# Optimization experiments

Measured on AMD Instinct MI355X. Metric: run time of the kernel, lower is better.

The kernel has to match this reference:

```python
import jax, jax.numpy as jnp
import numpy as np

ATT_DIM = 768
N_HEADS = 4
N_LABELS = 2000
NEG_INF = -1e6


def setup_inputs() -> dict:
    key = jax.random.key(0)
    k1, k2, k3, k4, k5, k6 = jax.random.split(key, 6)
    B, S, D = 4, 3072, ATT_DIM
    h = jax.random.normal(k1, (B, S, D), dtype=jnp.float32)
    attention_mask = jnp.ones((B, S), dtype=jnp.int32)
    label_feat = jax.random.normal(k2, (N_LABELS * N_HEADS, D), dtype=jnp.float32)
    # nn.Linear W: weight [D, D], bias [D]
    W_w = jax.random.normal(k3, (D, D), dtype=jnp.float32) * 0.02
    W_b = jnp.zeros((D,), dtype=jnp.float32)
    # classifier: weight [num_labels, D], bias [num_labels]
    cls_w = jax.random.normal(k4, (N_LABELS, D), dtype=jnp.float32) * 0.02
    cls_b = jnp.zeros((N_LABELS,), dtype=jnp.float32)
    return {"h": h, "attention_mask": attention_mask, "label_feat": label_feat,
            "W_w": W_w, "W_b": W_b, "cls_w": cls_w, "cls_b": cls_b}


def reference(h, attention_mask, label_feat, W_w, W_b, cls_w, cls_b):
    # h: [B,S,D]; label_feat: [E*H, D]
    B, S, D = h.shape
    E = label_feat.shape[0] // N_HEADS
    z = jnp.tanh(h @ W_w.T + W_b)                       # [B,S,D]
    u = label_feat.reshape(E, N_HEADS, D)               # [E,H,D]
    # score 'abd,ecd->aebc' -> [B,E,S,H]
    score = jnp.einsum('bsd,ehd->besh', z, u)
    mask = attention_mask.astype(bool)[:, None, :, None]  # [B,1,S,1]
    score = jnp.where(mask, score, NEG_INF)
    alpha = jax.nn.softmax(score, axis=2)               # softmax over seq
    # m 'abd,aebc->aedc' -> [B,E,D,H]
    m = jnp.einsum('bsd,besh->bedh', h, alpha)
    m = m.max(axis=-1)                                  # head max-pool -> [B,E,D]
    logits = jnp.sum(cls_w[None] * m, axis=2) + cls_b   # [B,E]
    return logits, m
```

## Files before the change

kernel.cpp:

```cpp
#include <hip/hip_runtime.h>
#include <hip/hip_bf16.h>

typedef _Float16 f16;
typedef _Float16 half8 __attribute__((ext_vector_type(8)));
typedef _Float16 half4v __attribute__((ext_vector_type(4)));
typedef float f32x4 __attribute__((ext_vector_type(4)));

#define B_ 4
#define S_ 3072
#define D_ 768
#define E_ 2000
#define NEG_INF -1.0e6f

#define GLD16(gsrc, ldst)                                                     \
  __builtin_amdgcn_global_load_lds(                                           \
      (const __attribute__((address_space(1))) void*)(gsrc),                  \
      (__attribute__((address_space(3))) void*)(ldst), 16, 0, 0)

__global__ __launch_bounds__(256) void k_transpose(const float* __restrict__ h,
                                                   f16* __restrict__ ht) {
  __shared__ f16 tile[64][65];
  int b = blockIdx.z, s0 = blockIdx.x * 64, d0 = blockIdx.y * 64;
  int t = threadIdx.x, tx = t & 63, ty = t >> 6;
  const float* src = h + ((size_t)b * S_ + s0) * D_ + d0;
#pragma unroll
  for (int i = 0; i < 16; ++i) {
    int sl = i * 4 + ty;
    tile[sl][tx] = (f16)src[(size_t)sl * D_ + tx];
  }
  __syncthreads();
  f16* dst = ht + ((size_t)b * D_ + d0) * S_ + s0;
#pragma unroll
  for (int i = 0; i < 16; ++i) {
    int dl = i * 4 + ty;
    dst[(size_t)dl * S_ + tx] = tile[tx][dl];
  }
}

__global__ __launch_bounds__(256) void k_zgemm(const float* __restrict__ h,
                                               const float* __restrict__ W,
                                               const float* __restrict__ bias,
                                               f16* __restrict__ zb) {
  __shared__ f16 As[64][40];
  __shared__ f16 Bs[64][40];
  int i0 = blockIdx.x * 64, j0 = blockIdx.y * 64;
  int t = threadIdx.x, w = t >> 6, lane = t & 63, g = lane >> 4, li = lane & 15;
  int wi = w >> 1, wj = w & 1;

  f32x4 acc[2][2];
#pragma unroll
  for (int a = 0; a < 2; ++a)
#pragma unroll
    for (int b2 = 0; b2 < 2; ++b2) acc[a][b2] = (f32x4){0.f, 0.f, 0.f, 0.f};

  int srow = t >> 2, scol = (t & 3) * 8;
  const float* pA = h + (size_t)(i0 + srow) * D_ + scol;
  const float* pB = W + (size_t)(j0 + srow) * D_ + scol;

  for (int kc = 0; kc < D_; kc += 32) {
    float4 a0 = *(const float4*)(pA + kc);
    float4 a1 = *(const float4*)(pA + kc + 4);
    float4 b0 = *(const float4*)(pB + kc);
    float4 b1 = *(const float4*)(pB + kc + 4);
    half8 av = {(f16)a0.x, (f16)a0.y, (f16)a0.z, (f16)a0.w,
                (f16)a1.x, (f16)a1.y, (f16)a1.z, (f16)a1.w};
    half8 bv = {(f16)b0.x, (f16)b0.y, (f16)b0.z, (f16)b0.w,
                (f16)b1.x, (f16)b1.y, (f16)b1.z, (f16)b1.w};
    *(half8*)&As[srow][scol] = av;
    *(half8*)&Bs[srow][scol] = bv;
    __syncthreads();
#pragma unroll
    for (int it = 0; it < 2; ++it) {
      half8 af = *(const half8*)&As[wi * 32 + it * 16 + li][g * 8];
#pragma unroll
      for (int jt = 0; jt < 2; ++jt) {
        half8 bf = *(const half8*)&Bs[wj * 32 + jt * 16 + li][g * 8];
        acc[it][jt] =
            __builtin_amdgcn_mfma_f32_16x16x32_f16(af, bf, acc[it][jt], 0, 0, 0);
      }
    }
    __syncthreads();
  }
#pragma unroll
  for (int it = 0; it < 2; ++it) {
#pragma unroll
    for (int jt = 0; jt < 2; ++jt) {
      int jj = j0 + wj * 32 + jt * 16 + li;
      float bsv = bias[jj];
#pragma unroll
      for (int r = 0; r < 4; ++r) {
        int ii = i0 + wi * 32 + it * 16 + g * 4 + r;
        float v = acc[it][jt][r] + bsv;
        zb[(size_t)ii * D_ + jj] = (f16)tanhf(v);
      }
    }
  }
}

__global__ __launch_bounds__(512, 1) void k_attn(const float* __restrict__ lf,
                                                 const f16* __restrict__ zb,
                                                 const f16* __restrict__ ht,
                                                 const int* __restrict__ amask,
                                                 float* __restrict__ out_m) {
  __shared__ f16 KsBuf[2][32 * 768];
  __shared__ f16 VsBuf[768 * 32];
  __shared__ f16 PtBuf[64 * 32];
  __shared__ float Cp[32][68];
  __shared__ float Fac[64];
  __shared__ float Lfin[64];
  __shared__ int Msk[2][32];

  char* KsB = (char*)&KsBuf[0][0];
  char* VsB = (char*)VsBuf;
  char* PtB = (char*)PtBuf;

  const int fid = blockIdx.x;
  const int x2 = fid & 7, u = fid >> 3;
  const int b = x2 >> 1;
  const int qtile = (x2 & 1) * 64 + u;
  if (qtile >= 125) return;
  const int q0 = qtile * 64;

  const int t = threadIdx.x, w = t >> 6, lane = t & 63;
  const int g = lane >> 4, li = lane & 15;
  const int qt = w & 3, kh = w >> 2;
  const int dh = w;

  half8 qf[12];
  {
    const float* qp = lf + (size_t)(q0 + qt * 16 + li) * D_ + kh * 384 + g * 8;
#pragma unroll
    for (int f = 0; f < 12; ++f) {
      float4 v0 = *(const float4*)(qp + f * 32);
      float4 v1 = *(const float4*)(qp + f * 32 + 4);
      qf[f] = (half8){(f16)v0.x, (f16)v0.y, (f16)v0.z, (f16)v0.w,
                      (f16)v1.x, (f16)v1.y, (f16)v1.z, (f16)v1.w};
    }
  }

  int klds[6], kgsw[6];
#pragma unroll
  for (int k = 0; k < 6; ++k) {
    int lin = (w * 6 + k) * 1024 + lane * 16;
    int row = lin / 1536;
    int xo = lin - row * 1536;
    klds[k] = lin;
    kgsw[k] = row * 1536 + (xo ^ ((row & 7) << 4));
  }
  int vlds[6], vgsw[6];
#pragma unroll
  for (int k = 0; k < 6; ++k) {
    int j = w * 6 + k;
    int vd = j * 16 + (lane >> 2);
    vlds[k] = j * 1024 + lane * 16;
    vgsw[k] = vd * (S_ * 2) + (((lane & 3) * 16) ^ ((vd & 3) << 4));
  }

  const int amask7 = (li & 7) << 4;
  const int arow0 = li * 1536 + kh * 768;
  const int arow1 = (16 + li) * 1536 + kh * 768;

  const int vroff = (dh * 96 + li) * 64 + ((g * 16) ^ ((li & 3) << 4));
  int ptoff[4];
#pragma unroll
  for (int qs = 0; qs < 4; ++qs)
    ptoff[qs] = (qs * 16 + li) * 64 + ((g * 16) ^ ((li & 3) << 4));

  const int pwoff0 = (qt * 16 + li) * 64 + ((g * 8) ^ ((li & 3) << 4));
  const int pwoff1 = (qt * 16 + li) * 64 + ((32 + g * 8) ^ ((li & 3) << 4));

  const char* zbB = (const char*)zb + (size_t)b * S_ * 1536;
  const char* htB = (const char*)ht + (size_t)b * D_ * S_ * 2;

#pragma unroll
  for (int k = 0; k < 6; ++k) GLD16(zbB + kgsw[k], KsB + klds[k]);
  if (t < 32) Msk[0][t] = amask[b * S_ + t];
  asm volatile("s_waitcnt vmcnt(0)" ::: "memory");
  __syncthreads();

  float mreg = -3.0e38f, lreg = 0.0f;
  f32x4 oacc[4][6];
#pragma unroll
  for (int a = 0; a < 4; ++a)
#pragma unroll
    for (int d = 0; d < 6; ++d) oacc[a][d] = (f32x4){0.f, 0.f, 0.f, 0.f};

  for (int i = 0; i < 96; ++i) {
    const int s0 = i * 32;
    const int s0n = (i < 95) ? s0 + 32 : 0;
    const int cur = i & 1, nxt = cur ^ 1;
    const char* ksC = KsB + cur * 49152;

    int mnext = (t < 32) ? amask[b * S_ + s0n + t] : 0;
    {
      const char* src = htB + (size_t)s0 * 2;
#pragma unroll
      for (int k = 0; k < 6; ++k) GLD16(src + vgsw[k], VsB + vlds[k]);
    }

    f32x4 c0 = {0.f, 0.f, 0.f, 0.f}, c1 = {0.f, 0.f, 0.f, 0.f};
    f32x4 e0 = {0.f, 0.f, 0.f, 0.f}, e1 = {0.f, 0.f, 0.f, 0.f};
    __builtin_amdgcn_s_setprio(1);
#pragma unroll
    for (int kf = 0; kf < 6; ++kf) {
      const int col = (kf * 64 + g * 16) ^ amask7;
      half8 a0 = *(const half8*)(ksC + arow0 + col);
      half8 a1 = *(const half8*)(ksC + arow1 + col);
      c0 = __builtin_amdgcn_mfma_f32_16x16x32_f16(a0, qf[kf], c0, 0, 0, 0);
      c1 = __builtin_amdgcn_mfma_f32_16x16x32_f16(a1, qf[kf], c1, 0, 0, 0);
    }
#pragma unroll
    for (int kf = 6; kf < 12; ++kf) {
      const int col = (kf * 64 + g * 16) ^ amask7;
      half8 a0 = *(const half8*)(ksC + arow0 + col);
      half8 a1 = *(const half8*)(ksC + arow1 + col);
      e0 = __builtin_amdgcn_mfma_f32_16x16x32_f16(a0, qf[kf], e0, 0, 0, 0);
      e1 = __builtin_amdgcn_mfma_f32_16x16x32_f16(a1, qf[kf], e1, 0, 0, 0);
    }
    __builtin_amdgcn_s_setprio(0);
    c0 = c0 + e0;
    c1 = c1 + e1;

    __builtin_amdgcn_sched_barrier(0);
    {
      const char* src = zbB + (size_t)s0n * 1536;
      char* dst = KsB + nxt * 49152;
#pragma unroll
      for (int k = 0; k < 6; ++k) GLD16(src + kgsw[k], dst + klds[k]);
    }

    if (kh == 1) {
#pragma unroll
      for (int r = 0; r < 4; ++r) {
        Cp[g * 4 + r][qt * 16 + li] = c0[r];
        Cp[16 + g * 4 + r][qt * 16 + li] = c1[r];
      }
    }
    __syncthreads();

    if (kh == 0) {
      const int* mk = Msk[i & 1];
      float p[8];
      float vmax = -3.0e38f;
#pragma unroll
      for (int r = 0; r < 4; ++r) {
        float sv0 = c0[r] + Cp[g * 4 + r][qt * 16 + li];
        float sv1 = c1[r] + Cp[16 + g * 4 + r][qt * 16 + li];
        if (!mk[g * 4 + r]) sv0 = NEG_INF;
        if (!mk[16 + g * 4 + r]) sv1 = NEG_INF;
        p[r] = sv0;
        p[4 + r] = sv1;
        vmax = fmaxf(vmax, fmaxf(sv0, sv1));
      }
      vmax = fmaxf(vmax, __shfl_xor(vmax, 16));
      vmax = fmaxf(vmax, __shfl_xor(vmax, 32));
      float Mn = fmaxf(mreg, vmax);
      float fec = __expf(mreg - Mn);
      mreg = Mn;
      float ts = 0.f;
#pragma unroll
      for (int r = 0; r < 8; ++r) {
        p[r] = __expf(p[r] - Mn);
        ts += p[r];
      }
      ts += __shfl_xor(ts, 16);
      ts += __shfl_xor(ts, 32);
      lreg = lreg * fec + ts;
      if (lane < 16) Fac[qt * 16 + li] = fec;
      *(half4v*)(PtB + pwoff0) =
          (half4v){(f16)p[0], (f16)p[1], (f16)p[2], (f16)p[3]};
      *(half4v*)(PtB + pwoff1) =
          (half4v){(f16)p[4], (f16)p[5], (f16)p[6], (f16)p[7]};
    }
    if (t < 32) Msk[(i + 1) & 1][t] = mnext;
    asm volatile("s_waitcnt vmcnt(6)" ::: "memory");
    __syncthreads();

    {
      float fr[4][4];
#pragma unroll
      for (int qs = 0; qs < 4; ++qs)
#pragma unroll
        for (int r = 0; r < 4; ++r) fr[qs][r] = Fac[qs * 16 + g * 4 + r];
#pragma unroll
      for (int qs = 0; qs < 4; ++qs)
#pragma unroll
        for (int dt = 0; dt < 6; ++dt)
#pragma unroll
          for (int r = 0; r < 4; ++r) oacc[qs][dt][r] *= fr[qs][r];
      half8 pa[4];
#pragma unroll
      for (int qs = 0; qs < 4; ++qs) pa[qs] = *(const half8*)(PtB + ptoff[qs]);
      __builtin_amdgcn_s_setprio(1);
#pragma unroll
      for (int dt = 0; dt < 6; ++dt) {
        half8 vb = *(const half8*)(VsB + vroff + dt * 1024);
#pragma unroll
        for (int qs = 0; qs < 4; ++qs)
          oacc[qs][dt] =
              __builtin_amdgcn_mfma_f32_16x16x32_f16(pa[qs], vb, oacc[qs][dt], 0, 0, 0);
      }
      __builtin_amdgcn_s_setprio(0);
    }
    asm volatile("s_waitcnt vmcnt(0)" ::: "memory");
    __syncthreads();
  }

  if (kh == 0 && lane < 16) Lfin[qt * 16 + li] = lreg;
  __syncthreads();

#pragma unroll
  for (int qs = 0; qs < 4; ++qs) {
    float rl[4];
#pragma unroll
    for (int r = 0; r < 4; ++r) rl[r] = 1.0f / Lfin[qs * 16 + g * 4 + r];
    int e_loc = qs * 4 + g;
    float* od = out_m + ((size_t)b * E_ + (q0 >> 2) + e_loc) * D_ + dh * 96 + li;
#pragma unroll
    for (int dt = 0; dt < 6; ++dt) {
      float mv = oacc[qs][dt][0] * rl[0];
      mv = fmaxf(mv, oacc[qs][dt][1] * rl[1]);
      mv = fmaxf(mv, oacc[qs][dt][2] * rl[2]);
      mv = fmaxf(mv, oacc[qs][dt][3] * rl[3]);
      od[dt * 16] = mv;
    }
  }
}

__global__ __launch_bounds__(256) void k_logits(const float* __restrict__ cw,
                                                const float* __restrict__ cb,
                                                const float* __restrict__ m,
                                                float* __restrict__ out) {
  int t = threadIdx.x, w = t >> 6, lane = t & 63;
  int rid = blockIdx.x * 4 + w;
  int b = rid / E_, e = rid - b * E_;
  const float* mr = m + (size_t)rid * D_;
  const float* cr = cw + (size_t)e * D_;
  float acc = 0.f;
#pragma unroll
  for (int i = 0; i < 12; ++i) acc += cr[i * 64 + lane] * mr[i * 64 + lane];
#pragma unroll
  for (int off = 32; off >= 1; off >>= 1) acc += __shfl_xor(acc, off);
  if (lane == 0) out[rid] = acc + cb[e];
}

extern "C" void kernel_launch(void* const* d_in, const int* in_sizes, int n_in,
                              void* d_out, int out_size, void* d_ws, size_t ws_size,
                              hipStream_t stream) {
  const float* h = (const float*)d_in[0];
  const int* amask = (const int*)d_in[1];
  const float* lf = (const float*)d_in[2];
  const float* Ww = (const float*)d_in[3];
  const float* Wb = (const float*)d_in[4];
  const float* cw = (const float*)d_in[5];
  const float* cb = (const float*)d_in[6];
  float* out = (float*)d_out;

  f16* zb = (f16*)d_ws;
  f16* ht = (f16*)((char*)d_ws + 18874368);

  k_transpose<<<dim3(48, 12, 4), 256, 0, stream>>>(h, ht);
  k_zgemm<<<dim3(192, 12), 256, 0, stream>>>(h, Ww, Wb, zb);
  k_attn<<<512, 512, 0, stream>>>(lf, zb, ht, amask, out + 8000);
  k_logits<<<2000, 256, 0, stream>>>(cw, cb, out + 8000, out);
}
```

Baseline: 633.3 us.

## Load V fragments directly into registers and software-pipeline PV with next QK

Removes the shared-memory V staging buffer and loads each warp's ht fragments straight from global memory into double-buffered registers. The loop is restructured so the P·V MFMA for the previous tile runs at the start of the next iteration, before that iteration's QK^T, with a final drain after the loop. This drops one barrier per iteration, replaces __syncthreads with raw s_barrier plus explicit waitcnt, and changes the P-buffer swizzle. The aim is to hide V load latency and cut LDS traffic and synchronisation, at the cost of more VGPRs and uncoalesced, strided global loads for V.

```diff
diff --git a/kernel.cpp b/kernel.cpp
--- a/kernel.cpp
+++ b/kernel.cpp
@@ -103,7 +103,6 @@
                                                  const int* __restrict__ amask,
                                                  float* __restrict__ out_m) {
   __shared__ f16 KsBuf[2][32 * 768];
-  __shared__ f16 VsBuf[768 * 32];
   __shared__ f16 PtBuf[64 * 32];
   __shared__ float Cp[32][68];
   __shared__ float Fac[64];
@@ -111,7 +110,6 @@
   __shared__ int Msk[2][32];
 
   char* KsB = (char*)&KsBuf[0][0];
-  char* VsB = (char*)VsBuf;
   char* PtB = (char*)PtBuf;
 
   const int fid = blockIdx.x;
@@ -147,30 +145,21 @@
     klds[k] = lin;
     kgsw[k] = row * 1536 + (xo ^ ((row & 7) << 4));
   }
-  int vlds[6], vgsw[6];
-#pragma unroll
-  for (int k = 0; k < 6; ++k) {
-    int j = w * 6 + k;
-    int vd = j * 16 + (lane >> 2);
-    vlds[k] = j * 1024 + lane * 16;
-    vgsw[k] = vd * (S_ * 2) + (((lane & 3) * 16) ^ ((vd & 3) << 4));
-  }
 
   const int amask7 = (li & 7) << 4;
   const int arow0 = li * 1536 + kh * 768;
   const int arow1 = (16 + li) * 1536 + kh * 768;
 
-  const int vroff = (dh * 96 + li) * 64 + ((g * 16) ^ ((li & 3) << 4));
+  const int pswz = ((li >> 1) & 3) << 4;
   int ptoff[4];
 #pragma unroll
   for (int qs = 0; qs < 4; ++qs)
-    ptoff[qs] = (qs * 16 + li) * 64 + ((g * 16) ^ ((li & 3) << 4));
-
-  const int pwoff0 = (qt * 16 + li) * 64 + ((g * 8) ^ ((li & 3) << 4));
-  const int pwoff1 = (qt * 16 + li) * 64 + ((32 + g * 8) ^ ((li & 3) << 4));
+    ptoff[qs] = (qs * 16 + li) * 64 + ((g * 16) ^ pswz);
+  const int pwoff0 = (qt * 16 + li) * 64 + ((g * 8) ^ pswz);
+  const int pwoff1 = (qt * 16 + li) * 64 + ((32 + g * 8) ^ pswz);
 
   const char* zbB = (const char*)zb + (size_t)b * S_ * 1536;
-  const char* htB = (const char*)ht + (size_t)b * D_ * S_ * 2;
+  const f16* vbase = ht + ((size_t)b * D_ + dh * 96 + li) * S_ + g * 8;
 
 #pragma unroll
   for (int k = 0; k < 6; ++k) GLD16(zbB + kgsw[k], KsB + klds[k]);
@@ -185,125 +174,139 @@
 #pragma unroll
     for (int d = 0; d < 6; ++d) oacc[a][d] = (f32x4){0.f, 0.f, 0.f, 0.f};
 
-  for (int i = 0; i < 96; ++i) {
-    const int s0 = i * 32;
-    const int s0n = (i < 95) ? s0 + 32 : 0;
-    const int cur = i & 1, nxt = cur ^ 1;
-    const char* ksC = KsB + cur * 49152;
-
-    int mnext = (t < 32) ? amask[b * S_ + s0n + t] : 0;
-    {
-      const char* src = htB + (size_t)s0 * 2;
-#pragma unroll
-      for (int k = 0; k < 6; ++k) GLD16(src + vgsw[k], VsB + vlds[k]);
-    }
-
-    f32x4 c0 = {0.f, 0.f, 0.f, 0.f}, c1 = {0.f, 0.f, 0.f, 0.f};
-    f32x4 e0 = {0.f, 0.f, 0.f, 0.f}, e1 = {0.f, 0.f, 0.f, 0.f};
-    __builtin_amdgcn_s_setprio(1);
-#pragma unroll
-    for (int kf = 0; kf < 6; ++kf) {
-      const int col = (kf * 64 + g * 16) ^ amask7;
-      half8 a0 = *(const half8*)(ksC + arow0 + col);
-      half8 a1 = *(const half8*)(ksC + arow1 + col);
-      c0 = __builtin_amdgcn_mfma_f32_16x16x32_f16(a0, qf[kf], c0, 0, 0, 0);
-      c1 = __builtin_amdgcn_mfma_f32_16x16x32_f16(a1, qf[kf], c1, 0, 0, 0);
-    }
-#pragma unroll
-    for (int kf = 6; kf < 12; ++kf) {
-      const int col = (kf * 64 + g * 16) ^ amask7;
-      half8 a0 = *(const half8*)(ksC + arow0 + col);
-      half8 a1 = *(const half8*)(ksC + arow1 + col);
-      e0 = __builtin_amdgcn_mfma_f32_16x16x32_f16(a0, qf[kf], e0, 0, 0, 0);
-      e1 = __builtin_amdgcn_mfma_f32_16x16x32_f16(a1, qf[kf], e1, 0, 0, 0);
-    }
-    __builtin_amdgcn_s_setprio(0);
-    c0 = c0 + e0;
-    c1 = c1 + e1;
-
-    __builtin_amdgcn_sched_barrier(0);
-    {
-      const char* src = zbB + (size_t)s0n * 1536;
-      char* dst = KsB + nxt * 49152;
-#pragma unroll
-      for (int k = 0; k < 6; ++k) GLD16(src + kgsw[k], dst + klds[k]);
-    }
-
-    if (kh == 1) {
-#pragma unroll
-      for (int r = 0; r < 4; ++r) {
-        Cp[g * 4 + r][qt * 16 + li] = c0[r];
-        Cp[16 + g * 4 + r][qt * 16 + li] = c1[r];
-      }
-    }
-    __syncthreads();
-
-    if (kh == 0) {
-      const int* mk = Msk[i & 1];
-      float p[8];
-      float vmax = -3.0e38f;
-#pragma unroll
-      for (int r = 0; r < 4; ++r) {
-        float sv0 = c0[r] + Cp[g * 4 + r][qt * 16 + li];
-        float sv1 = c1[r] + Cp[16 + g * 4 + r][qt * 16 + li];
-        if (!mk[g * 4 + r]) sv0 = NEG_INF;
-        if (!mk[16 + g * 4 + r]) sv1 = NEG_INF;
-        p[r] = sv0;
-        p[4 + r] = sv1;
-        vmax = fmaxf(vmax, fmaxf(sv0, sv1));
-      }
-      vmax = fmaxf(vmax, __shfl_xor(vmax, 16));
-      vmax = fmaxf(vmax, __shfl_xor(vmax, 32));
-      float Mn = fmaxf(mreg, vmax);
-      float fec = __expf(mreg - Mn);
-      mreg = Mn;
-      float ts = 0.f;
-#pragma unroll
-      for (int r = 0; r < 8; ++r) {
-        p[r] = __expf(p[r] - Mn);
-        ts += p[r];
-      }
-      ts += __shfl_xor(ts, 16);
-      ts += __shfl_xor(ts, 32);
-      lreg = lreg * fec + ts;
-      if (lane < 16) Fac[qt * 16 + li] = fec;
-      *(half4v*)(PtB + pwoff0) =
-          (half4v){(f16)p[0], (f16)p[1], (f16)p[2], (f16)p[3]};
-      *(half4v*)(PtB + pwoff1) =
-          (half4v){(f16)p[4], (f16)p[5], (f16)p[6], (f16)p[7]};
-    }
-    if (t < 32) Msk[(i + 1) & 1][t] = mnext;
-    asm volatile("s_waitcnt vmcnt(6)" ::: "memory");
-    __syncthreads();
-
-    {
-      float fr[4][4];
+  half8 Vb0[6], Vb1[6];
+
+#define ATT_BODY(I_, VRD, VWR)                                                \
+  {                                                                           \
+    const int i_ = (I_);                                                      \
+    const int s0_ = i_ * 32;                                                  \
+    const int s0n_ = (i_ < 95) ? s0_ + 32 : 0;                                \
+    const char* ksC_ = KsB + (i_ & 1) * 49152;                                \
+    char* ksN_ = KsB + ((i_ & 1) ^ 1) * 49152;                                \
+    int mnext_ = (t < 32) ? amask[b * S_ + s0n_ + t] : 0;                     \
+    {                            \
+      const char* src_ = zbB + (size_t)s0n_ * 1536;                           \
+      _Pragma("unroll") for (int k = 0; k < 6; ++k)                           \
+          GLD16(src_ + kgsw[k], ksN_ + klds[k]);                              \
+    }                                                                         \
+    {                         \
+      const f16* vp_ = vbase + s0_;                                           \
+      _Pragma("unroll") for (int dt = 0; dt < 6; ++dt)                        \
+          VWR[dt] = *(const half8*)(vp_ + (size_t)dt * 16 * S_);              \
+    }                                                                         \
+    __builtin_amdgcn_sched_barrier(0);                                        \
+    if (i_ > 0) {                       \
+      float fr_[4][4];                                                        \
+      _Pragma("unroll") for (int qs = 0; qs < 4; ++qs)                        \
+          _Pragma("unroll") for (int r = 0; r < 4; ++r)                       \
+              fr_[qs][r] = Fac[qs * 16 + g * 4 + r];                          \
+      _Pragma("unroll") for (int qs = 0; qs < 4; ++qs)                        \
+          _Pragma("unroll") for (int dt = 0; dt < 6; ++dt)                    \
+              _Pragma("unroll") for (int r = 0; r < 4; ++r)                   \
+                  oacc[qs][dt][r] *= fr_[qs][r];                              \
+      half8 pa_[4];                                                           \
+      _Pragma("unroll") for (int qs = 0; qs < 4; ++qs)                        \
+          pa_[qs] = *(const half8*)(PtB + ptoff[qs]);                         \
+      __builtin_amdgcn_s_setprio(1);                                          \
+      _Pragma("unroll") for (int dt = 0; dt < 6; ++dt)                        \
+          _Pragma("unroll") for (int qs = 0; qs < 4; ++qs)                    \
+              oacc[qs][dt] = __builtin_amdgcn_mfma_f32_16x16x32_f16(          \
+                  pa_[qs], VRD[dt], oacc[qs][dt], 0, 0, 0);                   \
+      __builtin_amdgcn_s_setprio(0);                                          \
+    }                                                                         \
+                            \
+    f32x4 c0_ = {0.f, 0.f, 0.f, 0.f}, c1_ = {0.f, 0.f, 0.f, 0.f};             \
+    f32x4 e0_ = {0.f, 0.f, 0.f, 0.f}, e1_ = {0.f, 0.f, 0.f, 0.f};             \
+    __builtin_amdgcn_s_setprio(1);                                            \
+    _Pragma("unroll") for (int kf = 0; kf < 6; ++kf) {                        \
+      const int col = (kf * 64 + g * 16) ^ amask7;                            \
+      half8 a0 = *(const half8*)(ksC_ + arow0 + col);                         \
+      half8 a1 = *(const half8*)(ksC_ + arow1 + col);                         \
+      c0_ = __builtin_amdgcn_mfma_f32_16x16x32_f16(a0, qf[kf], c0_, 0, 0, 0); \
+      c1_ = __builtin_amdgcn_mfma_f32_16x16x32_f16(a1, qf[kf], c1_, 0, 0, 0); \
+    }                                                                         \
+    _Pragma("unroll") for (int kf = 6; kf < 12; ++kf) {                       \
+      const int col = (kf * 64 + g * 16) ^ amask7;                            \
+      half8 a0 = *(const half8*)(ksC_ + arow0 + col);                         \
+      half8 a1 = *(const half8*)(ksC_ + arow1 + col);                         \
+      e0_ = __builtin_amdgcn_mfma_f32_16x16x32_f16(a0, qf[kf], e0_, 0, 0, 0); \
+      e1_ = __builtin_amdgcn_mfma_f32_16x16x32_f16(a1, qf[kf], e1_, 0, 0, 0); \
+    }                                                                         \
+    __builtin_amdgcn_s_setprio(0);                                            \
+    c0_ = c0_ + e0_;                                                          \
+    c1_ = c1_ + e1_;                                                          \
+    if (kh == 1) {                                                            \
+      _Pragma("unroll") for (int r = 0; r < 4; ++r) {                         \
+        Cp[g * 4 + r][qt * 16 + li] = c0_[r];                                 \
+        Cp[16 + g * 4 + r][qt * 16 + li] = c1_[r];                            \
+      }                                                                       \
+    }                                                                         \
+    asm volatile("s_waitcnt lgkmcnt(0)" ::: "memory");                        \
+    __builtin_amdgcn_s_barrier();                                  \
+    if (kh == 0) {                                                            \
+      const int* mk_ = Msk[i_ & 1];                                           \
+      float p_[8];                                                            \
+      float vmax_ = -3.0e38f;                                                 \
+      _Pragma("unroll") for (int r = 0; r < 4; ++r) {                         \
+        float sv0 = c0_[r] + Cp[g * 4 + r][qt * 16 + li];                     \
+        float sv1 = c1_[r] + Cp[16 + g * 4 + r][qt * 16 + li];                \
+        if (!mk_[g * 4 + r]) sv0 = NEG_INF;                                   \
+        if (!mk_[16 + g * 4 + r]) sv1 = NEG_INF;                              \
+        p_[r] = sv0;                                                          \
+        p_[4 + r] = sv1;                                                      \
+        vmax_ = fmaxf(vmax_, fmaxf(sv0, sv1));                                \
+      }                                                                       \
+      vmax_ = fmaxf(vmax_, __shfl_xor(vmax_, 16));                            \
+      vmax_ = fmaxf(vmax_, __shfl_xor(vmax_, 32));                            \
+      float Mn_ = fmaxf(mreg, vmax_);                                         \
+      float fec_ = __expf(mreg - Mn_);                                        \
+      mreg = Mn_;                                                             \
+      float ts_ = 0.f;                                                        \
+      _Pragma("unroll") for (int r = 0; r < 8; ++r) {                         \
+        p_[r] = __expf(p_[r] - Mn_);                                          \
+        ts_ += p_[r];                                                         \
+      }                                                                       \
+      ts_ += __shfl_xor(ts_, 16);                                             \
+      ts_ += __shfl_xor(ts_, 32);                                             \
+      lreg = lreg * fec_ + ts_;                                               \
+      if (lane < 16) Fac[qt * 16 + li] = fec_;                                \
+      *(half4v*)(PtB + pwoff0) =                                              \
+          (half4v){(f16)p_[0], (f16)p_[1], (f16)p_[2], (f16)p_[3]};           \
+      *(half4v*)(PtB + pwoff1) =                                              \
+          (half4v){(f16)p_[4], (f16)p_[5], (f16)p_[6], (f16)p_[7]};           \
+    }                                                                         \
+    if (t < 32) Msk[(i_ + 1) & 1][t] = mnext_;                                \
+    asm volatile("s_waitcnt vmcnt(6) lgkmcnt(0)" ::: "memory");               \
+    __builtin_amdgcn_s_barrier();             \
+  }
+
+  for (int ii = 0; ii < 96; ii += 2) {
+    ATT_BODY(ii, Vb1, Vb0)
+    ATT_BODY(ii + 1, Vb0, Vb1)
+  }
+#undef ATT_BODY
+
+  {
+    float fr_[4][4];
+#pragma unroll
+    for (int qs = 0; qs < 4; ++qs)
+#pragma unroll
+      for (int r = 0; r < 4; ++r) fr_[qs][r] = Fac[qs * 16 + g * 4 + r];
+#pragma unroll
+    for (int qs = 0; qs < 4; ++qs)
+#pragma unroll
+      for (int dt = 0; dt < 6; ++dt)
+#pragma unroll
+        for (int r = 0; r < 4; ++r) oacc[qs][dt][r] *= fr_[qs][r];
+    half8 pa_[4];
+#pragma unroll
+    for (int qs = 0; qs < 4; ++qs) pa_[qs] = *(const half8*)(PtB + ptoff[qs]);
+#pragma unroll
+    for (int dt = 0; dt < 6; ++dt)
 #pragma unroll
       for (int qs = 0; qs < 4; ++qs)
-#pragma unroll
-        for (int r = 0; r < 4; ++r) fr[qs][r] = Fac[qs * 16 + g * 4 + r];
-#pragma unroll
-      for (int qs = 0; qs < 4; ++qs)
-#pragma unroll
-        for (int dt = 0; dt < 6; ++dt)
-#pragma unroll
-          for (int r = 0; r < 4; ++r) oacc[qs][dt][r] *= fr[qs][r];
-      half8 pa[4];
-#pragma unroll
-      for (int qs = 0; qs < 4; ++qs) pa[qs] = *(const half8*)(PtB + ptoff[qs]);
-      __builtin_amdgcn_s_setprio(1);
-#pragma unroll
-      for (int dt = 0; dt < 6; ++dt) {
-        half8 vb = *(const half8*)(VsB + vroff + dt * 1024);
-#pragma unroll
-        for (int qs = 0; qs < 4; ++qs)
-          oacc[qs][dt] =
-              __builtin_amdgcn_mfma_f32_16x16x32_f16(pa[qs], vb, oacc[qs][dt], 0, 0, 0);
-      }
-      __builtin_amdgcn_s_setprio(0);
-    }
-    asm volatile("s_waitcnt vmcnt(0)" ::: "memory");
-    __syncthreads();
+        oacc[qs][dt] = __builtin_amdgcn_mfma_f32_16x16x32_f16(
+            pa_[qs], Vb1[dt], oacc[qs][dt], 0, 0, 0);
   }
 
   if (kh == 0 && lane < 16) Lfin[qt * 16 + li] = lreg;
```

New measurement: 1.067 ms. 68.6% more time.
